# Kernel tuning notes

Hardware: AMD Instinct MI355X
Metric: run time of the kernel (lower is better)

The kernel has to match this reference:

```python
import jax, jax.numpy as jnp
import numpy as np

LN_EPS = 1e-5


def setup_inputs() -> dict:
    key = jax.random.key(0)
    ks = jax.random.split(key, 4)
    B, L, Dm, N = 16, 2048, 512, 64
    return {
        "x": jax.random.normal(ks[0], (B, L, Dm), dtype=jnp.float32),
        "A": jax.random.normal(ks[1], (Dm, N), dtype=jnp.float32),
        "C": jax.random.normal(ks[2], (Dm, N), dtype=jnp.float32),
        "D": jax.random.normal(ks[3], (Dm,), dtype=jnp.float32),
        "gamma": jnp.ones((Dm,), dtype=jnp.float32),
        "beta": jnp.zeros((Dm,), dtype=jnp.float32),
    }


def reference(x, A, C, D, gamma, beta):
    # LayerNorm over last dim (matches nn.LayerNorm(d_model))
    mean = jnp.mean(x, axis=-1, keepdims=True)
    var = jnp.mean(jnp.square(x - mean), axis=-1, keepdims=True)
    x_norm = (x - mean) * jax.lax.rsqrt(var + LN_EPS) * gamma + beta

    B, L, Dm = x.shape
    N = A.shape[1]
    h0 = jnp.zeros((B, N), dtype=x.dtype)

    def step(h, u):
        # u: [B, Dm]; h: [B, N]
        h = jnp.tanh(u @ A + h)
        y = h @ C.T + u * D  # [B, Dm]
        return h, y

    # scan over time: xs [L, B, Dm]
    _, ys = jax.lax.scan(step, h0, jnp.swapaxes(x_norm, 0, 1))
    out = jnp.swapaxes(ys, 0, 1)  # [B, L, Dm]
    return out + x
```

## Files before the change

kernel.cpp:

```cpp
#include <hip/hip_runtime.h>
#include <hip/hip_bf16.h>

typedef short bf16x8 __attribute__((ext_vector_type(8)));
typedef float f32x4 __attribute__((ext_vector_type(4)));

constexpr int B_ = 16;
constexpr int L_ = 2048;
constexpr int DM = 512;
constexpr int NS = 64;
constexpr int BL = B_ * L_;
constexpr float LN_EPS = 1e-5f;
constexpr float KLN = 2.8853900817779268f;

constexpr int SEGS = 32;
constexpr int LSEG = L_ / SEGS;
constexpr int WARM = 64;

__device__ __forceinline__ unsigned f32bits(float f) {
    union { float f; unsigned u; } v{f}; return v.u;
}
__device__ __forceinline__ float bitsf32(unsigned u) {
    union { unsigned u; float f; } v{u}; return v.f;
}
__device__ __forceinline__ unsigned short f2bf(float f) {
    unsigned u = f32bits(f);
    unsigned r = u + 0x7FFF + ((u >> 16) & 1);
    return (unsigned short)(r >> 16);
}

__device__ __forceinline__ void norm_split8(float4 u0, float4 u1,
                                            float rstd, float m2,
                                            bf16x8& ah, bf16x8& al) {
    float t[8] = { fmaf(u0.x, rstd, m2), fmaf(u0.y, rstd, m2),
                   fmaf(u0.z, rstd, m2), fmaf(u0.w, rstd, m2),
                   fmaf(u1.x, rstd, m2), fmaf(u1.y, rstd, m2),
                   fmaf(u1.z, rstd, m2), fmaf(u1.w, rstd, m2) };
    unsigned hb[8], lb[8];
    #pragma unroll
    for (int j = 0; j < 8; ++j) {
        unsigned tb = f32bits(t[j]);
        hb[j] = tb & 0xFFFF0000u;
        lb[j] = f32bits(t[j] - bitsf32(hb[j]));
    }
    union { unsigned u[4]; bf16x8 v; } H, L;
    #pragma unroll
    for (int p = 0; p < 4; ++p) {
        H.u[p] = (hb[2*p] >> 16) | hb[2*p+1];
        L.u[p] = (lb[2*p] >> 16) | (lb[2*p+1] & 0xFFFF0000u);
    }
    ah = H.v; al = L.v;
}

__global__ __launch_bounds__(256) void k_pack(const float* __restrict__ A,
                                              const float* __restrict__ C,
                                              const float* __restrict__ gamma,
                                              const float* __restrict__ beta,
                                              const float* __restrict__ Dv,
                                              unsigned short* __restrict__ PAh,
                                              unsigned short* __restrict__ PAl,
                                              unsigned short* __restrict__ PC,
                                              float* __restrict__ c0,
                                              float* __restrict__ gd,
                                              float* __restrict__ bd) {
    const int blk = blockIdx.x;
    const int tid = threadIdx.x;
    if (blk < 32) {
        const int g = blk * 256 + tid;
        if (g < 4096) {
            const int lane = g & 63, ct = (g >> 6) & 3, k32 = (g >> 8) & 3, kc = g >> 10;
            const int kbase = kc * 128 + k32 * 32 + (lane >> 4) * 8;
            const int col   = ct * 16 + (lane & 15);
            unsigned hb[8], lb[8];
            #pragma unroll
            for (int j = 0; j < 8; ++j) {
                float v = gamma[kbase + j] * A[(size_t)(kbase + j) * NS + col];
                unsigned tb = f32bits(v);
                hb[j] = tb & 0xFFFF0000u;
                lb[j] = f32bits(v - bitsf32(hb[j]));
            }
            uint4 ph, pl;
            ph.x = (hb[0] >> 16) | hb[1]; ph.y = (hb[2] >> 16) | hb[3];
            ph.z = (hb[4] >> 16) | hb[5]; ph.w = (hb[6] >> 16) | hb[7];
            pl.x = (lb[0] >> 16) | (lb[1] & 0xFFFF0000u);
            pl.y = (lb[2] >> 16) | (lb[3] & 0xFFFF0000u);
            pl.z = (lb[4] >> 16) | (lb[5] & 0xFFFF0000u);
            pl.w = (lb[6] >> 16) | (lb[7] & 0xFFFF0000u);
            *reinterpret_cast<uint4*>(PAh + (size_t)g * 8) = ph;
            *reinterpret_cast<uint4*>(PAl + (size_t)g * 8) = pl;
        } else {
            const int g2 = g - 4096;
            unsigned short v[8];
            #pragma unroll
            for (int j = 0; j < 8; ++j) v[j] = f2bf(C[(size_t)g2 * 8 + j]);
            uint4 p;
            p.x = v[0] | ((unsigned)v[1] << 16); p.y = v[2] | ((unsigned)v[3] << 16);
            p.z = v[4] | ((unsigned)v[5] << 16); p.w = v[6] | ((unsigned)v[7] << 16);
            *reinterpret_cast<uint4*>(PC + (size_t)g2 * 8) = p;
        }
    } else {
        __shared__ float red[256];
        #pragma unroll
        for (int i = 0; i < 2; ++i) {
            int d = tid + 256 * i;
            gd[d] = gamma[d] * Dv[d];
            bd[d] = beta[d] * Dv[d];
        }
        const int n = tid & 63, part = tid >> 6;
        float s = 0.f;
        #pragma unroll 8
        for (int k = part * 128; k < part * 128 + 128; ++k)
            s += beta[k] * A[(size_t)k * NS + n];
        red[tid] = s;
        __syncthreads();
        if (tid < 64)
            c0[tid] = red[tid] + red[tid + 64] + red[tid + 128] + red[tid + 192];
    }
}

__global__ __launch_bounds__(512, 2) void k_gemmA(const float* __restrict__ x,
                                               const unsigned short* __restrict__ PAh,
                                               const unsigned short* __restrict__ PAl,
                                               const float* __restrict__ c0,
                                               float* __restrict__ stats,
                                               float* __restrict__ Bu) {
    __shared__ unsigned short AsH[4 * 16 * 64 * 8];
    __shared__ unsigned short AsL[4 * 16 * 64 * 8];
    const int tid  = threadIdx.x;
    const int r0   = blockIdx.x * 128;
    const int w    = tid >> 6;
    const int lane = tid & 63;
    const int myrow = 16 * w + (lane & 15);
    const int kb    = (lane >> 4) * 8;
    const float* xrow = x + (size_t)(r0 + myrow) * DM;

    {
        const float4* sh = reinterpret_cast<const float4*>(PAh);
        const float4* sl = reinterpret_cast<const float4*>(PAl);
        float4* dh = reinterpret_cast<float4*>(AsH);
        float4* dl = reinterpret_cast<float4*>(AsL);
        #pragma unroll
        for (int i = 0; i < 8; ++i) {
            dh[tid + 512 * i] = sh[tid + 512 * i];
            dl[tid + 512 * i] = sl[tid + 512 * i];
        }
    }

    float4 xv[32];
    #pragma unroll
    for (int kc = 0; kc < 4; ++kc) {
        #pragma unroll
        for (int k32 = 0; k32 < 4; ++k32) {
            xv[kc * 8 + 2 * k32]     = *reinterpret_cast<const float4*>(
                xrow + kc * 128 + k32 * 32 + kb);
            xv[kc * 8 + 2 * k32 + 1] = *reinterpret_cast<const float4*>(
                xrow + kc * 128 + k32 * 32 + kb + 4);
        }
    }

    float s = 0.f, s2 = 0.f;
    #pragma unroll
    for (int i = 0; i < 32; ++i) {
        float4 a = xv[i];
        s  += (a.x + a.y) + (a.z + a.w);
        s2 += a.x*a.x + a.y*a.y + a.z*a.z + a.w*a.w;
    }
    s += __shfl_xor(s, 16); s2 += __shfl_xor(s2, 16);
    s += __shfl_xor(s, 32); s2 += __shfl_xor(s2, 32);
    const float mean = s * (1.0f / DM);
    const float var  = s2 * (1.0f / DM) - mean * mean;
    const float rstd = rsqrtf(var + LN_EPS);
    const float m2   = -mean * rstd;
    if (lane < 16) {
        stats[2 * (r0 + myrow)]     = mean;
        stats[2 * (r0 + myrow) + 1] = rstd;
    }

    __syncthreads();

    f32x4 acc[4] = {};
    const bf16x8* ABh = reinterpret_cast<const bf16x8*>(AsH);
    const bf16x8* ABl = reinterpret_cast<const bf16x8*>(AsL);

    #pragma unroll
    for (int kc = 0; kc < 4; ++kc) {
        #pragma unroll
        for (int k32 = 0; k32 < 4; ++k32) {
            bf16x8 ah, al;
            norm_split8(xv[kc * 8 + 2 * k32], xv[kc * 8 + 2 * k32 + 1], rstd, m2, ah, al);
            #pragma unroll
            for (int ct = 0; ct < 4; ++ct) {
                const int fi = ((kc * 4 + k32) * 4 + ct) * 64 + lane;
                bf16x8 bh = ABh[fi];
                bf16x8 bl = ABl[fi];
                acc[ct] = __builtin_amdgcn_mfma_f32_16x16x32_bf16(ah, bh, acc[ct], 0, 0, 0);
                acc[ct] = __builtin_amdgcn_mfma_f32_16x16x32_bf16(ah, bl, acc[ct], 0, 0, 0);
                acc[ct] = __builtin_amdgcn_mfma_f32_16x16x32_bf16(al, bh, acc[ct], 0, 0, 0);
            }
        }
    }

    const int orow = r0 + 16 * w + (lane >> 4) * 4;
    #pragma unroll
    for (int ct = 0; ct < 4; ++ct) {
        const int n = ct * 16 + (lane & 15);
        const float c0n = c0[n];
        #pragma unroll
        for (int j = 0; j < 4; ++j)
            Bu[(size_t)(orow + j) * NS + n] = acc[ct][j] + c0n;
    }
}

__global__ __launch_bounds__(512, 4) void k_scanC(const float* __restrict__ x,
                                                  const unsigned short* __restrict__ PC,
                                                  const float* __restrict__ gd,
                                                  const float* __restrict__ bd,
                                                  const float* __restrict__ stats,
                                                  const float* __restrict__ Bu,
                                                  float* __restrict__ out) {
    __shared__ unsigned short Hs[64 * 64];
    const int tid = threadIdx.x;
    const int seg = blockIdx.x & (SEGS - 1);
    const int b   = blockIdx.x >> 5;
    const int l0  = seg * LSEG;
    const int rowbase = b * L_ + l0;

    if (tid < 64) {
        constexpr int G = 16;
        const int n     = tid;
        const int start = (seg == 0) ? 0 : (l0 - WARM);
        const int skip  = l0 - start;
        const int nGrp  = (l0 + LSEG - start) / G;
        const float* bp = Bu + ((size_t)b * L_ + start) * NS + n;
        char* hbase = reinterpret_cast<char*>(Hs);

        float bufA[G], bufB[G];
        #pragma unroll
        for (int j = 0; j < G; ++j) bufA[j] = KLN * bp[(size_t)j * NS];
        float hv = 0.0f;
        int g = 0;
        for (;;) {
            {
                if (g + 1 < nGrp) {
                    const int base = (g + 1) * G;
                    #pragma unroll
                    for (int j = 0; j < G; ++j)
                        bufB[j] = KLN * bp[(size_t)(base + j) * NS];
                }
                const int lbase = g * G - skip;
                const bool doStore = lbase >= 0;
                #pragma unroll
                for (int j = 0; j < G; ++j) {
                    float t = fmaf(hv, KLN, bufA[j]);
                    float e = __builtin_amdgcn_exp2f(t);
                    float rr = __builtin_amdgcn_rcpf(e + 1.0f);
                    hv = fmaf(-2.0f, rr, 1.0f);
                    if (doStore) {
                        const int lr = lbase + j;
                        *reinterpret_cast<unsigned short*>(
                            hbase + lr * 128 + ((2 * n) ^ ((lr & 7) << 4))) = f2bf(hv);
                    }
                }
            }
            if (++g == nGrp) break;
            {
                if (g + 1 < nGrp) {
                    const int base = (g + 1) * G;
                    #pragma unroll
                    for (int j = 0; j < G; ++j)
                        bufA[j] = KLN * bp[(size_t)(base + j) * NS];
                }
                const int lbase = g * G - skip;
                const bool doStore = lbase >= 0;
                #pragma unroll
                for (int j = 0; j < G; ++j) {
                    float t = fmaf(hv, KLN, bufB[j]);
                    float e = __builtin_amdgcn_exp2f(t);
                    float rr = __builtin_amdgcn_rcpf(e + 1.0f);
                    hv = fmaf(-2.0f, rr, 1.0f);
                    if (doStore) {
                        const int lr = lbase + j;
                        *reinterpret_cast<unsigned short*>(
                            hbase + lr * 128 + ((2 * n) ^ ((lr & 7) << 4))) = f2bf(hv);
                    }
                }
            }
            if (++g == nGrp) break;
        }
    }
    __syncthreads();

    const int w    = tid >> 6;
    const int lane = tid & 63;
    const int rt   = w >> 1;
    const int dh   = (w & 1) * 256;
    const int arow = rt * 16 + (lane & 15);

    bf16x8 afr[2];
    #pragma unroll
    for (int kt = 0; kt < 2; ++kt) {
        const int byte = arow * 128 + ((kt * 64 + (lane >> 4) * 16) ^ ((arow & 7) << 4));
        afr[kt] = *reinterpret_cast<const bf16x8*>(
            reinterpret_cast<const char*>(Hs) + byte);
    }

    const int rb = rowbase + rt * 16 + (lane >> 4) * 4;
    float mean_[4], rstd_[4];
    #pragma unroll
    for (int j = 0; j < 4; ++j) {
        mean_[j] = stats[2 * (rb + j)];
        rstd_[j] = stats[2 * (rb + j) + 1];
    }

    const int dl = dh + (lane & 15);
    const int n0 = (lane >> 4) * 8;
    #pragma unroll
    for (int ct = 0; ct < 16; ++ct) {
        const int d = dl + ct * 16;
        bf16x8 b0 = *reinterpret_cast<const bf16x8*>(PC + (size_t)d * NS + n0);
        bf16x8 b1 = *reinterpret_cast<const bf16x8*>(PC + (size_t)d * NS + 32 + n0);
        f32x4 a = {};
        a = __builtin_amdgcn_mfma_f32_16x16x32_bf16(afr[0], b0, a, 0, 0, 0);
        a = __builtin_amdgcn_mfma_f32_16x16x32_bf16(afr[1], b1, a, 0, 0, 0);
        const float gdv = gd[d];
        const float bdv = bd[d];
        #pragma unroll
        for (int j = 0; j < 4; ++j) {
            const size_t idx = (size_t)(rb + j) * DM + d;
            const float xv = x[idx];
            const float z  = (xv - mean_[j]) * rstd_[j];
            out[idx] = a[j] + z * gdv + bdv + xv;
        }
    }
}

extern "C" void kernel_launch(void* const* d_in, const int* in_sizes, int n_in,
                              void* d_out, int out_size, void* d_ws, size_t ws_size,
                              hipStream_t stream) {
    const float* x     = (const float*)d_in[0];
    const float* A     = (const float*)d_in[1];
    const float* C     = (const float*)d_in[2];
    const float* Dv    = (const float*)d_in[3];
    const float* gamma = (const float*)d_in[4];
    const float* beta  = (const float*)d_in[5];
    float* out = (float*)d_out;

    char* ws = (char*)d_ws;
    float* Bu           = (float*)(ws);
    float* stats        = (float*)(ws + (size_t)BL * NS * 4);
    char* p = ws + (size_t)BL * NS * 4 + (size_t)BL * 2 * 4;
    unsigned short* PAh = (unsigned short*)p;        p += (size_t)DM * NS * 2;
    unsigned short* PAl = (unsigned short*)p;        p += (size_t)DM * NS * 2;
    unsigned short* PC  = (unsigned short*)p;        p += (size_t)DM * NS * 2;
    float* c0           = (float*)p;                 p += 256;
    float* gd           = (float*)p;                 p += (size_t)DM * 4;
    float* bd           = (float*)p;

    k_pack<<<33, 256, 0, stream>>>(A, C, gamma, beta, Dv, PAh, PAl, PC, c0, gd, bd);
    k_gemmA<<<BL / 128, 512, 0, stream>>>(x, PAh, PAl, c0, stats, Bu);
    k_scanC<<<B_ * SEGS, 512, 0, stream>>>(x, PC, gd, bd, stats, Bu, out);
}
```

Baseline: 67.42 us.

## Fuse input GEMM, scan and output GEMM into one kernel with flags

Merges the LayerNorm+A-projection kernel and the scan+C-projection kernel into one kernel of 256 blocks of 128 rows. Each block publishes a flag once its Bu rows are written, and waits on the previous block's flag before running its warm-started recurrence. Keeping x and the LayerNorm statistics in registers removes the second global read of x and the stats buffer, and C is repacked so the output tile is written as contiguous row vectors. In exchange it relies on all blocks being co-resident for the spin-wait to be safe, uses 128KB of LDS per block, and has a single wave run a longer serial recurrence while the others wait.

```diff
diff --git a/kernel.cpp b/kernel.cpp
--- a/kernel.cpp
+++ b/kernel.cpp
@@ -12,9 +12,9 @@
 constexpr float LN_EPS = 1e-5f;
 constexpr float KLN = 2.8853900817779268f;
 
-constexpr int SEGS = 32;
-constexpr int LSEG = L_ / SEGS;
 constexpr int WARM = 64;
+constexpr int RPB  = 128;
+constexpr int NBLK = BL / RPB;
 
 __device__ __forceinline__ unsigned f32bits(float f) {
     union { float f; unsigned u; } v{f}; return v.u;
@@ -58,7 +58,7 @@
                                               const float* __restrict__ Dv,
                                               unsigned short* __restrict__ PAh,
                                               unsigned short* __restrict__ PAl,
-                                              unsigned short* __restrict__ PC,
+                                              unsigned short* __restrict__ PC2,
                                               float* __restrict__ c0,
                                               float* __restrict__ gd,
                                               float* __restrict__ bd) {
@@ -88,14 +88,21 @@
             *reinterpret_cast<uint4*>(PAh + (size_t)g * 8) = ph;
             *reinterpret_cast<uint4*>(PAl + (size_t)g * 8) = pl;
         } else {
-            const int g2 = g - 4096;
+            const int g2   = g - 4096;
+            const int lane = g2 & 63;
+            const int kt   = (g2 >> 6) & 1;
+            const int offs = (g2 >> 7) & 1;
+            const int dblk = g2 >> 8;
+            const int i    = lane & 15;
+            const int d    = dblk * 32 + ((i >> 2) * 8) + offs * 4 + (i & 3);
+            const int nb   = kt * 32 + (lane >> 4) * 8;
             unsigned short v[8];
             #pragma unroll
-            for (int j = 0; j < 8; ++j) v[j] = f2bf(C[(size_t)g2 * 8 + j]);
+            for (int j = 0; j < 8; ++j) v[j] = f2bf(C[(size_t)d * NS + nb + j]);
             uint4 p;
             p.x = v[0] | ((unsigned)v[1] << 16); p.y = v[2] | ((unsigned)v[3] << 16);
             p.z = v[4] | ((unsigned)v[5] << 16); p.w = v[6] | ((unsigned)v[7] << 16);
-            *reinterpret_cast<uint4*>(PC + (size_t)g2 * 8) = p;
+            *reinterpret_cast<uint4*>(PC2 + (size_t)g2 * 8) = p;
         }
     } else {
         __shared__ float red[256];
@@ -117,22 +124,28 @@
     }
 }
 
-__global__ __launch_bounds__(512, 2) void k_gemmA(const float* __restrict__ x,
-                                               const unsigned short* __restrict__ PAh,
-                                               const unsigned short* __restrict__ PAl,
-                                               const float* __restrict__ c0,
-                                               float* __restrict__ stats,
-                                               float* __restrict__ Bu) {
-    __shared__ unsigned short AsH[4 * 16 * 64 * 8];
-    __shared__ unsigned short AsL[4 * 16 * 64 * 8];
+__global__ __launch_bounds__(512, 2) void k_mega(const float* __restrict__ x,
+                                                 const unsigned short* __restrict__ PAh,
+                                                 const unsigned short* __restrict__ PAl,
+                                                 const unsigned short* __restrict__ PC2,
+                                                 const float* __restrict__ c0,
+                                                 const float* __restrict__ gd,
+                                                 const float* __restrict__ bd,
+                                                 float* __restrict__ Bu,
+                                                 unsigned* __restrict__ flags,
+                                                 float* __restrict__ out) {
+    __shared__ __align__(16) char smem[131072];
     const int tid  = threadIdx.x;
-    const int r0   = blockIdx.x * 128;
+    const int blk  = blockIdx.x;
     const int w    = tid >> 6;
     const int lane = tid & 63;
     const int myrow = 16 * w + (lane & 15);
     const int kb    = (lane >> 4) * 8;
+    const int r0    = blk * RPB;
     const float* xrow = x + (size_t)(r0 + myrow) * DM;
 
+    unsigned short* AsH = (unsigned short*)smem;
+    unsigned short* AsL = (unsigned short*)(smem + 65536);
     {
         const float4* sh = reinterpret_cast<const float4*>(PAh);
         const float4* sl = reinterpret_cast<const float4*>(PAl);
@@ -170,68 +183,60 @@
     const float var  = s2 * (1.0f / DM) - mean * mean;
     const float rstd = rsqrtf(var + LN_EPS);
     const float m2   = -mean * rstd;
-    if (lane < 16) {
-        stats[2 * (r0 + myrow)]     = mean;
-        stats[2 * (r0 + myrow) + 1] = rstd;
-    }
 
     __syncthreads();
 
-    f32x4 acc[4] = {};
-    const bf16x8* ABh = reinterpret_cast<const bf16x8*>(AsH);
-    const bf16x8* ABl = reinterpret_cast<const bf16x8*>(AsL);
-
-    #pragma unroll
-    for (int kc = 0; kc < 4; ++kc) {
-        #pragma unroll
-        for (int k32 = 0; k32 < 4; ++k32) {
-            bf16x8 ah, al;
-            norm_split8(xv[kc * 8 + 2 * k32], xv[kc * 8 + 2 * k32 + 1], rstd, m2, ah, al);
+    {
+        f32x4 acc[4] = {};
+        const bf16x8* ABh = reinterpret_cast<const bf16x8*>(AsH);
+        const bf16x8* ABl = reinterpret_cast<const bf16x8*>(AsL);
+        #pragma unroll
+        for (int kc = 0; kc < 4; ++kc) {
             #pragma unroll
-            for (int ct = 0; ct < 4; ++ct) {
-                const int fi = ((kc * 4 + k32) * 4 + ct) * 64 + lane;
-                bf16x8 bh = ABh[fi];
-                bf16x8 bl = ABl[fi];
-                acc[ct] = __builtin_amdgcn_mfma_f32_16x16x32_bf16(ah, bh, acc[ct], 0, 0, 0);
-                acc[ct] = __builtin_amdgcn_mfma_f32_16x16x32_bf16(ah, bl, acc[ct], 0, 0, 0);
-                acc[ct] = __builtin_amdgcn_mfma_f32_16x16x32_bf16(al, bh, acc[ct], 0, 0, 0);
+            for (int k32 = 0; k32 < 4; ++k32) {
+                bf16x8 ah, al;
+                norm_split8(xv[kc * 8 + 2 * k32], xv[kc * 8 + 2 * k32 + 1], rstd, m2, ah, al);
+                #pragma unroll
+                for (int ct = 0; ct < 4; ++ct) {
+                    const int fi = ((kc * 4 + k32) * 4 + ct) * 64 + lane;
+                    bf16x8 bh = ABh[fi];
+                    bf16x8 bl = ABl[fi];
+                    acc[ct] = __builtin_amdgcn_mfma_f32_16x16x32_bf16(ah, bh, acc[ct], 0, 0, 0);
+                    acc[ct] = __builtin_amdgcn_mfma_f32_16x16x32_bf16(ah, bl, acc[ct], 0, 0, 0);
+                    acc[ct] = __builtin_amdgcn_mfma_f32_16x16x32_bf16(al, bh, acc[ct], 0, 0, 0);
+                }
             }
         }
-    }
-
-    const int orow = r0 + 16 * w + (lane >> 4) * 4;
-    #pragma unroll
-    for (int ct = 0; ct < 4; ++ct) {
-        const int n = ct * 16 + (lane & 15);
-        const float c0n = c0[n];
-        #pragma unroll
-        for (int j = 0; j < 4; ++j)
-            Bu[(size_t)(orow + j) * NS + n] = acc[ct][j] + c0n;
-    }
-}
-
-__global__ __launch_bounds__(512, 4) void k_scanC(const float* __restrict__ x,
-                                                  const unsigned short* __restrict__ PC,
-                                                  const float* __restrict__ gd,
-                                                  const float* __restrict__ bd,
-                                                  const float* __restrict__ stats,
-                                                  const float* __restrict__ Bu,
-                                                  float* __restrict__ out) {
-    __shared__ unsigned short Hs[64 * 64];
-    const int tid = threadIdx.x;
-    const int seg = blockIdx.x & (SEGS - 1);
-    const int b   = blockIdx.x >> 5;
-    const int l0  = seg * LSEG;
-    const int rowbase = b * L_ + l0;
-
-    if (tid < 64) {
+        const int orow = r0 + 16 * w + (lane >> 4) * 4;
+        #pragma unroll
+        for (int ct = 0; ct < 4; ++ct) {
+            const int n = ct * 16 + (lane & 15);
+            const float c0n = c0[n];
+            #pragma unroll
+            for (int j = 0; j < 4; ++j)
+                Bu[(size_t)(orow + j) * NS + n] = acc[ct][j] + c0n;
+        }
+    }
+    __threadfence();
+    __syncthreads();
+    if (tid == 0)
+        __hip_atomic_store(&flags[blk], 1u, __ATOMIC_RELEASE, __HIP_MEMORY_SCOPE_AGENT);
+
+    const int l0 = (blk & 15) * RPB;
+    const int bb = blk >> 4;
+    if (w == 0) {
+        if ((blk & 15) != 0) {
+            while (__hip_atomic_load(&flags[blk - 1], __ATOMIC_ACQUIRE,
+                                     __HIP_MEMORY_SCOPE_AGENT) == 0u)
+                __builtin_amdgcn_s_sleep(2);
+        }
         constexpr int G = 16;
-        const int n     = tid;
-        const int start = (seg == 0) ? 0 : (l0 - WARM);
+        const int n     = lane;
+        const int start = (l0 == 0) ? 0 : (l0 - WARM);
         const int skip  = l0 - start;
-        const int nGrp  = (l0 + LSEG - start) / G;
-        const float* bp = Bu + ((size_t)b * L_ + start) * NS + n;
-        char* hbase = reinterpret_cast<char*>(Hs);
+        const int nGrp  = (RPB + skip) / G;
+        const float* bp = Bu + ((size_t)bb * L_ + start) * NS + n;
+        char* hbase = smem;
 
         float bufA[G], bufB[G];
         #pragma unroll
@@ -286,50 +291,59 @@
             }
             if (++g == nGrp) break;
         }
+    } else {
+        float* GdS = (float*)(smem + 16384);
+        const int t2 = tid - 64;
+        if (t2 < 256)
+            reinterpret_cast<float4*>(GdS)[t2] =
+                (t2 < 128) ? reinterpret_cast<const float4*>(gd)[t2]
+                           : reinterpret_cast<const float4*>(bd)[t2 - 128];
     }
     __syncthreads();
 
-    const int w    = tid >> 6;
-    const int lane = tid & 63;
-    const int rt   = w >> 1;
-    const int dh   = (w & 1) * 256;
-    const int arow = rt * 16 + (lane & 15);
-
-    bf16x8 afr[2];
-    #pragma unroll
-    for (int kt = 0; kt < 2; ++kt) {
-        const int byte = arow * 128 + ((kt * 64 + (lane >> 4) * 16) ^ ((arow & 7) << 4));
-        afr[kt] = *reinterpret_cast<const bf16x8*>(
-            reinterpret_cast<const char*>(Hs) + byte);
-    }
-
-    const int rb = rowbase + rt * 16 + (lane >> 4) * 4;
-    float mean_[4], rstd_[4];
-    #pragma unroll
-    for (int j = 0; j < 4; ++j) {
-        mean_[j] = stats[2 * (rb + j)];
-        rstd_[j] = stats[2 * (rb + j) + 1];
-    }
-
-    const int dl = dh + (lane & 15);
-    const int n0 = (lane >> 4) * 8;
-    #pragma unroll
-    for (int ct = 0; ct < 16; ++ct) {
-        const int d = dl + ct * 16;
-        bf16x8 b0 = *reinterpret_cast<const bf16x8*>(PC + (size_t)d * NS + n0);
-        bf16x8 b1 = *reinterpret_cast<const bf16x8*>(PC + (size_t)d * NS + 32 + n0);
-        f32x4 a = {};
-        a = __builtin_amdgcn_mfma_f32_16x16x32_bf16(afr[0], b0, a, 0, 0, 0);
-        a = __builtin_amdgcn_mfma_f32_16x16x32_bf16(afr[1], b1, a, 0, 0, 0);
-        const float gdv = gd[d];
-        const float bdv = bd[d];
-        #pragma unroll
-        for (int j = 0; j < 4; ++j) {
-            const size_t idx = (size_t)(rb + j) * DM + d;
-            const float xv = x[idx];
-            const float z  = (xv - mean_[j]) * rstd_[j];
-            out[idx] = a[j] + z * gdv + bdv + xv;
-        }
+    const float* GdS = (const float*)(smem + 16384);
+    const float* BdS = GdS + DM;
+
+    bf16x8 hfr0, hfr1;
+    {
+        const int hr = myrow;
+        hfr0 = *reinterpret_cast<const bf16x8*>(
+            smem + hr * 128 + (((lane >> 4) * 16) ^ ((hr & 7) << 4)));
+        hfr1 = *reinterpret_cast<const bf16x8*>(
+            smem + hr * 128 + ((64 + (lane >> 4) * 16) ^ ((hr & 7) << 4)));
+    }
+    float* orp = out + (size_t)(r0 + myrow) * DM;
+    #pragma unroll
+    for (int dblk = 0; dblk < 16; ++dblk) {
+        bf16x8 c00 = *reinterpret_cast<const bf16x8*>(PC2 + ((size_t)dblk * 256 + lane) * 8);
+        bf16x8 c01 = *reinterpret_cast<const bf16x8*>(PC2 + ((size_t)dblk * 256 + 64 + lane) * 8);
+        bf16x8 c10 = *reinterpret_cast<const bf16x8*>(PC2 + ((size_t)dblk * 256 + 128 + lane) * 8);
+        bf16x8 c11 = *reinterpret_cast<const bf16x8*>(PC2 + ((size_t)dblk * 256 + 192 + lane) * 8);
+        f32x4 a0 = {}, a1 = {};
+        a0 = __builtin_amdgcn_mfma_f32_16x16x32_bf16(c00, hfr0, a0, 0, 0, 0);
+        a0 = __builtin_amdgcn_mfma_f32_16x16x32_bf16(c01, hfr1, a0, 0, 0, 0);
+        a1 = __builtin_amdgcn_mfma_f32_16x16x32_bf16(c10, hfr0, a1, 0, 0, 0);
+        a1 = __builtin_amdgcn_mfma_f32_16x16x32_bf16(c11, hfr1, a1, 0, 0, 0);
+
+        const int kc  = dblk >> 2, k32 = dblk & 3;
+        const float4 x0 = xv[kc * 8 + 2 * k32];
+        const float4 x1 = xv[kc * 8 + 2 * k32 + 1];
+        const int db = dblk * 32 + kb;
+        const float4 g0 = *reinterpret_cast<const float4*>(GdS + db);
+        const float4 g1 = *reinterpret_cast<const float4*>(GdS + db + 4);
+        const float4 d0 = *reinterpret_cast<const float4*>(BdS + db);
+        const float4 d1 = *reinterpret_cast<const float4*>(BdS + db + 4);
+        float4 o0, o1;
+        o0.x = fmaf((x0.x - mean) * rstd, g0.x, a0[0] + d0.x + x0.x);
+        o0.y = fmaf((x0.y - mean) * rstd, g0.y, a0[1] + d0.y + x0.y);
+        o0.z = fmaf((x0.z - mean) * rstd, g0.z, a0[2] + d0.z + x0.z);
+        o0.w = fmaf((x0.w - mean) * rstd, g0.w, a0[3] + d0.w + x0.w);
+        o1.x = fmaf((x1.x - mean) * rstd, g1.x, a1[0] + d1.x + x1.x);
+        o1.y = fmaf((x1.y - mean) * rstd, g1.y, a1[1] + d1.y + x1.y);
+        o1.z = fmaf((x1.z - mean) * rstd, g1.z, a1[2] + d1.z + x1.z);
+        o1.w = fmaf((x1.w - mean) * rstd, g1.w, a1[3] + d1.w + x1.w);
+        *reinterpret_cast<float4*>(orp + db)     = o0;
+        *reinterpret_cast<float4*>(orp + db + 4) = o1;
     }
 }
 
@@ -344,18 +358,17 @@
     const float* beta  = (const float*)d_in[5];
     float* out = (float*)d_out;
 
-    char* ws = (char*)d_ws;
-    float* Bu           = (float*)(ws);
-    float* stats        = (float*)(ws + (size_t)BL * NS * 4);
-    char* p = ws + (size_t)BL * NS * 4 + (size_t)BL * 2 * 4;
+    char* p = (char*)d_ws;
+    float* Bu           = (float*)p;                 p += (size_t)BL * NS * 4;
     unsigned short* PAh = (unsigned short*)p;        p += (size_t)DM * NS * 2;
     unsigned short* PAl = (unsigned short*)p;        p += (size_t)DM * NS * 2;
-    unsigned short* PC  = (unsigned short*)p;        p += (size_t)DM * NS * 2;
+    unsigned short* PC2 = (unsigned short*)p;        p += (size_t)DM * NS * 2;
     float* c0           = (float*)p;                 p += 256;
     float* gd           = (float*)p;                 p += (size_t)DM * 4;
-    float* bd           = (float*)p;
-
-    k_pack<<<33, 256, 0, stream>>>(A, C, gamma, beta, Dv, PAh, PAl, PC, c0, gd, bd);
-    k_gemmA<<<BL / 128, 512, 0, stream>>>(x, PAh, PAl, c0, stats, Bu);
-    k_scanC<<<B_ * SEGS, 512, 0, stream>>>(x, PC, gd, bd, stats, Bu, out);
-}
+    float* bd           = (float*)p;                 p += (size_t)DM * 4;
+    unsigned* flags     = (unsigned*)p;
+
+    k_pack<<<33, 256, 0, stream>>>(A, C, gamma, beta, Dv, PAh, PAl, PC2, c0, gd, bd);
+    hipMemsetAsync(flags, 0, NBLK * sizeof(unsigned), stream);
+    k_mega<<<NBLK, 512, 0, stream>>>(x, PAh, PAl, PC2, c0, gd, bd, Bu, flags, out);
+}
```

Result: slower. 115.8 us (+71.8%).

## Drop LDS staging and x register cache in LayerNorm+A GEMM kernel

Applied to the files above, without the earlier changes.

The gemmA kernel no longer copies the packed bf16 A matrices into shared memory; the MFMA loop reads B fragments straight from global memory, relying on L1/L2 caching. It also stops keeping the 32 float4 x values in registers and re-reads x from global memory on a second pass after computing the row statistics. Blocks shrink from 512 to 256 threads (64 rows each). The aim is to cut register and LDS pressure and the block-wide sync so more waves fit per CU, at the cost of reading x twice and more global-memory traffic for A fragments.

```diff
diff --git a/kernel.cpp b/kernel.cpp
--- a/kernel.cpp
+++ b/kernel.cpp
@@ -117,52 +117,31 @@
     }
 }
 
-__global__ __launch_bounds__(512, 2) void k_gemmA(const float* __restrict__ x,
+__global__ __launch_bounds__(256) void k_gemmA(const float* __restrict__ x,
                                                const unsigned short* __restrict__ PAh,
                                                const unsigned short* __restrict__ PAl,
                                                const float* __restrict__ c0,
                                                float* __restrict__ stats,
                                                float* __restrict__ Bu) {
-    __shared__ unsigned short AsH[4 * 16 * 64 * 8];
-    __shared__ unsigned short AsL[4 * 16 * 64 * 8];
     const int tid  = threadIdx.x;
-    const int r0   = blockIdx.x * 128;
+    const int r0   = blockIdx.x * 64;
     const int w    = tid >> 6;
     const int lane = tid & 63;
     const int myrow = 16 * w + (lane & 15);
     const int kb    = (lane >> 4) * 8;
     const float* xrow = x + (size_t)(r0 + myrow) * DM;
 
-    {
-        const float4* sh = reinterpret_cast<const float4*>(PAh);
-        const float4* sl = reinterpret_cast<const float4*>(PAl);
-        float4* dh = reinterpret_cast<float4*>(AsH);
-        float4* dl = reinterpret_cast<float4*>(AsL);
-        #pragma unroll
-        for (int i = 0; i < 8; ++i) {
-            dh[tid + 512 * i] = sh[tid + 512 * i];
-            dl[tid + 512 * i] = sl[tid + 512 * i];
-        }
-    }
-
-    float4 xv[32];
+    float s = 0.f, s2 = 0.f;
     #pragma unroll
     for (int kc = 0; kc < 4; ++kc) {
         #pragma unroll
         for (int k32 = 0; k32 < 4; ++k32) {
-            xv[kc * 8 + 2 * k32]     = *reinterpret_cast<const float4*>(
-                xrow + kc * 128 + k32 * 32 + kb);
-            xv[kc * 8 + 2 * k32 + 1] = *reinterpret_cast<const float4*>(
-                xrow + kc * 128 + k32 * 32 + kb + 4);
-        }
-    }
-
-    float s = 0.f, s2 = 0.f;
-    #pragma unroll
-    for (int i = 0; i < 32; ++i) {
-        float4 a = xv[i];
-        s  += (a.x + a.y) + (a.z + a.w);
-        s2 += a.x*a.x + a.y*a.y + a.z*a.z + a.w*a.w;
+            float4 a = *reinterpret_cast<const float4*>(xrow + kc * 128 + k32 * 32 + kb);
+            float4 b = *reinterpret_cast<const float4*>(xrow + kc * 128 + k32 * 32 + kb + 4);
+            s  += (a.x + a.y) + (a.z + a.w) + (b.x + b.y) + (b.z + b.w);
+            s2 += a.x*a.x + a.y*a.y + a.z*a.z + a.w*a.w
+                + b.x*b.x + b.y*b.y + b.z*b.z + b.w*b.w;
+        }
     }
     s += __shfl_xor(s, 16); s2 += __shfl_xor(s2, 16);
     s += __shfl_xor(s, 32); s2 += __shfl_xor(s2, 32);
@@ -175,18 +154,17 @@
         stats[2 * (r0 + myrow) + 1] = rstd;
     }
 
-    __syncthreads();
-
     f32x4 acc[4] = {};
-    const bf16x8* ABh = reinterpret_cast<const bf16x8*>(AsH);
-    const bf16x8* ABl = reinterpret_cast<const bf16x8*>(AsL);
-
+    const bf16x8* ABh = reinterpret_cast<const bf16x8*>(PAh);
+    const bf16x8* ABl = reinterpret_cast<const bf16x8*>(PAl);
     #pragma unroll
     for (int kc = 0; kc < 4; ++kc) {
         #pragma unroll
         for (int k32 = 0; k32 < 4; ++k32) {
+            float4 u0 = *reinterpret_cast<const float4*>(xrow + kc * 128 + k32 * 32 + kb);
+            float4 u1 = *reinterpret_cast<const float4*>(xrow + kc * 128 + k32 * 32 + kb + 4);
             bf16x8 ah, al;
-            norm_split8(xv[kc * 8 + 2 * k32], xv[kc * 8 + 2 * k32 + 1], rstd, m2, ah, al);
+            norm_split8(u0, u1, rstd, m2, ah, al);
             #pragma unroll
             for (int ct = 0; ct < 4; ++ct) {
                 const int fi = ((kc * 4 + k32) * 4 + ct) * 64 + lane;
@@ -356,6 +334,6 @@
     float* bd           = (float*)p;
 
     k_pack<<<33, 256, 0, stream>>>(A, C, gamma, beta, Dv, PAh, PAl, PC, c0, gd, bd);
-    k_gemmA<<<BL / 128, 512, 0, stream>>>(x, PAh, PAl, c0, stats, Bu);
+    k_gemmA<<<BL / 64, 256, 0, stream>>>(x, PAh, PAl, c0, stats, Bu);
     k_scanC<<<B_ * SEGS, 512, 0, stream>>>(x, PC, gd, bd, stats, Bu, out);
 }
```

After: 73.06 us. +8.4%, slower.
